# Optimization experiments

Measured on AMD Instinct MI355X. Metric: run time of the kernel, lower is better.

Reference implementation:

```python
import jax, jax.numpy as jnp
import numpy as np

# DPLayer config (init kwargs)
MAX_OP = False            # False -> min-plus (shortest path) semiring; null = +inf
MAKE_POS = True           # GraphLayer make_pos: force positive edge weights
NULL = -1e30 if MAX_OP else 1e30   # finite stand-in for +/-inf (grad-safe)
B, H, W = 512, 256, 256


def setup_inputs() -> dict:
    key = jax.random.key(0)
    images = jax.random.normal(key, (B, 1, H, W), dtype=jnp.float32)
    return {"images": images}


def _edge_weights(images):
    # GraphLayer: edge_f('euclidean') on pixel values, made positive via softplus.
    x = images[:, 0, :, :]                       # [B, H, W] node/edge costs theta
    if MAKE_POS:
        x = jax.nn.softplus(x)
    return x


def _dp(theta):
    # V[i,j] = theta[i,j] + comb(V[i-1,j], V[i-1,j-1], V[i,j-1]); comb = min (max_op=False)
    # Row recurrence is solved in parallel via prefix-sum + associative running-min:
    #   A[j] = comb(V[i-1,j], V[i-1,j-1])
    #   V[i,j] = S[j] + runmin_{k<=j}(A[k] - S[k-1]),  S = cumsum(theta row)
    comb = jnp.maximum if MAX_OP else jnp.minimum
    null = jnp.asarray(NULL, theta.dtype)
    b = theta.shape[0]

    v0 = jnp.cumsum(theta[:, 0, :], axis=-1)     # first row: only right moves

    def row_step(vprev, th_row):                 # vprev: [B,W], th_row: [B,W]
        shifted = jnp.concatenate([jnp.full((b, 1), null, theta.dtype), vprev[:, :-1]], axis=1)
        A = comb(vprev, shifted)                 # best of up / up-left
        S = jnp.cumsum(th_row, axis=-1)
        Sprev = jnp.concatenate([jnp.zeros((b, 1), theta.dtype), S[:, :-1]], axis=1)
        V = S + jax.lax.associative_scan(comb, A - Sprev, axis=-1)
        return V, None

    vlast, _ = jax.lax.scan(row_step, v0, jnp.moveaxis(theta[:, 1:, :], 1, 0))
    return vlast[:, -1]                          # path length to (H-1, W-1), [B]


def reference(images):
    theta = _edge_weights(images)
    fake_lengths = _dp(theta)
    return fake_lengths
```

## Files before the change

### kernel.cpp

```cpp
#include <hip/hip_runtime.h>


#define HH 256
#define WW 256
#define CH 8
#define NCH 32
#define NULLV 1e30f

#define SBAR() __builtin_amdgcn_sched_barrier(0)

template<int CTRL, int ROWM>
__device__ __forceinline__ float dpp_mov(float x, float oldv) {
    return __builtin_bit_cast(float, __builtin_amdgcn_update_dpp(
        __builtin_bit_cast(int, oldv), __builtin_bit_cast(int, x),
        CTRL, ROWM, 0xF, false));
}

__device__ __forceinline__ float wave_iscan_add(float x) {
    x += dpp_mov<0x111, 0xF>(x, 0.0f);
    x += dpp_mov<0x112, 0xF>(x, 0.0f);
    x += dpp_mov<0x114, 0xF>(x, 0.0f);
    x += dpp_mov<0x118, 0xF>(x, 0.0f);
    x += dpp_mov<0x142, 0xA>(x, 0.0f);
    x += dpp_mov<0x143, 0xC>(x, 0.0f);
    return x;
}

__device__ __forceinline__ float wave_iscan_min(float x) {
    x = fminf(x, dpp_mov<0x111, 0xF>(x, NULLV));
    x = fminf(x, dpp_mov<0x112, 0xF>(x, NULLV));
    x = fminf(x, dpp_mov<0x114, 0xF>(x, NULLV));
    x = fminf(x, dpp_mov<0x118, 0xF>(x, NULLV));
    x = fminf(x, dpp_mov<0x142, 0xA>(x, NULLV));
    x = fminf(x, dpp_mov<0x143, 0xC>(x, NULLV));
    return x;
}

__device__ __forceinline__ float softplus_f(float x) {
    float ax = fabsf(x);
    float t  = __expf(-ax);
    return fmaxf(x, 0.0f) + __logf(1.0f + t);
}

__device__ __forceinline__ float4 prep_row(float4 c) {
    float t0 = softplus_f(c.x);
    float t1 = t0 + softplus_f(c.y);
    float t2 = t1 + softplus_f(c.z);
    float t3 = t2 + softplus_f(c.w);
    float s    = wave_iscan_add(t3);
    float soff = dpp_mov<0x138, 0xF>(s, 0.0f);
    return make_float4(soff + t0, soff + t1, soff + t2, soff + t3);
}

template<int NR>
__device__ __forceinline__ void prep_run(const float4* gp, int row0,
                                         float* b0, float* b1, int lane) {
    float4 L0, L1, L2;
    L0 = gp[(size_t)(row0 + 0) * 64];
    if constexpr (NR > 1) L1 = gp[(size_t)(row0 + 1) * 64];
    if constexpr (NR > 2) L2 = gp[(size_t)(row0 + 2) * 64];
    SBAR();
    for (int k = 0; k < NCH; ++k) {
        float4 N0 = L0, N1 = L1, N2 = L2;
        if (k + 1 < NCH) {
            const size_t rn = (size_t)(k + 1) * CH + row0;
            N0 = gp[(rn + 0) * 64];
            if constexpr (NR > 1) N1 = gp[(rn + 1) * 64];
            if constexpr (NR > 2) N2 = gp[(rn + 2) * 64];
        }
        SBAR();
        float* buf = (k & 1) ? b1 : b0;
        *reinterpret_cast<float4*>(&buf[0 * WW + lane * 4]) = prep_row(L0);
        if constexpr (NR > 1)
            *reinterpret_cast<float4*>(&buf[1 * WW + lane * 4]) = prep_row(L1);
        if constexpr (NR > 2)
            *reinterpret_cast<float4*>(&buf[2 * WW + lane * 4]) = prep_row(L2);
        __syncthreads();
        L0 = N0; L1 = N1; L2 = N2;
    }
}

__global__ __launch_bounds__(512, 1) void dp_kernel(const float* __restrict__ img,
                                                    float* __restrict__ out) {
    const int tid = threadIdx.x;
    const int wid = tid >> 6;
    const int lane = tid & 63;

    __shared__ __align__(16) float sbuf[2][2][CH][WW];

    if (wid < 2) {
        const int imgi = wid;
        __builtin_amdgcn_s_setprio(1);
        float v0, v1, v2, v3;

        auto row_step = [&](const float4& S) {
            float soff = dpp_mov<0x138, 0xF>(S.w, 0.0f);
            float vm1  = dpp_mov<0x138, 0xF>(v3, NULLV);
            float B0 = fminf(v0, vm1) - soff;
            float B1 = fminf(v1, v0) - S.x;
            float B2 = fminf(v2, v1) - S.y;
            float B3 = fminf(v3, v2) - S.z;
            float m1 = fminf(B0, B1);
            float m2 = fminf(m1, B2);
            float m3 = fminf(m2, B3);
            float mm   = wave_iscan_min(m3);
            float moff = dpp_mov<0x138, 0xF>(mm, NULLV);
            v0 = S.x + fminf(moff, B0);
            v1 = S.y + fminf(moff, m1);
            v2 = S.z + fminf(moff, m2);
            v3 = S.w + fminf(moff, m3);
        };

#define RD(buf, i) (*reinterpret_cast<const float4*>(&(buf)[i][lane * 4]))
        __syncthreads();
        {
            const float(*buf)[WW] = sbuf[imgi][0];
            float4 R0 = RD(buf, 0), R1 = RD(buf, 1), R2 = RD(buf, 2),
                   R3 = RD(buf, 3), R4 = RD(buf, 4), R5 = RD(buf, 5),
                   R6 = RD(buf, 6), R7 = RD(buf, 7);
            v0 = R0.x; v1 = R0.y; v2 = R0.z; v3 = R0.w;
            row_step(R1); row_step(R2); row_step(R3); row_step(R4);
            row_step(R5); row_step(R6); row_step(R7);
        }
        for (int k = 1; k < NCH; ++k) {
            __syncthreads();
            const float(*buf)[WW] = sbuf[imgi][k & 1];
            float4 R0 = RD(buf, 0), R1 = RD(buf, 1), R2 = RD(buf, 2),
                   R3 = RD(buf, 3), R4 = RD(buf, 4), R5 = RD(buf, 5),
                   R6 = RD(buf, 6), R7 = RD(buf, 7);
            row_step(R0); row_step(R1); row_step(R2); row_step(R3);
            row_step(R4); row_step(R5); row_step(R6); row_step(R7);
        }
#undef RD
        if (lane == 63) out[2 * blockIdx.x + imgi] = v3;
    } else {
        const int imgi = (wid - 2) & 1;
        const int pw   = (wid - 2) >> 1;
        const float* gbase = img + (size_t)(2 * blockIdx.x + imgi) * HH * WW;
        const float4* gp = reinterpret_cast<const float4*>(gbase) + lane;
        const int row0 = pw * 3;
        float* b0 = &sbuf[imgi][0][row0][0];
        float* b1 = &sbuf[imgi][1][row0][0];
        if (pw < 2) prep_run<3>(gp, row0, b0, b1, lane);
        else        prep_run<2>(gp, row0, b0, b1, lane);
    }
}

extern "C" void kernel_launch(void* const* d_in, const int* in_sizes, int n_in,
                              void* d_out, int out_size, void* d_ws, size_t ws_size,
                              hipStream_t stream) {
    const float* img = (const float*)d_in[0];
    float* out = (float*)d_out;
    dp_kernel<<<out_size / 2, 512, 0, stream>>>(img, out);
}
```

Baseline: 45.19 us.

## Enlarge DP row chunks to 32 rows and software-pipeline LDS reads

```diff
diff --git a/kernel.cpp b/kernel.cpp
--- a/kernel.cpp
+++ b/kernel.cpp
@@ -3,8 +3,8 @@
 
 #define HH 256
 #define WW 256
-#define CH 8
-#define NCH 32
+#define CH 32
+#define NCH 8
 #define NULLV 1e30f
 
 #define SBAR() __builtin_amdgcn_sched_barrier(0)
@@ -55,28 +55,27 @@
 template<int NR>
 __device__ __forceinline__ void prep_run(const float4* gp, int row0,
                                          float* b0, float* b1, int lane) {
-    float4 L0, L1, L2;
-    L0 = gp[(size_t)(row0 + 0) * 64];
-    if constexpr (NR > 1) L1 = gp[(size_t)(row0 + 1) * 64];
-    if constexpr (NR > 2) L2 = gp[(size_t)(row0 + 2) * 64];
+    float4 L[NR];
+#pragma unroll
+    for (int i = 0; i < NR; ++i) L[i] = gp[(size_t)(row0 + i) * 64];
     SBAR();
     for (int k = 0; k < NCH; ++k) {
-        float4 N0 = L0, N1 = L1, N2 = L2;
+        float4 N[NR];
+#pragma unroll
+        for (int i = 0; i < NR; ++i) N[i] = L[i];
         if (k + 1 < NCH) {
             const size_t rn = (size_t)(k + 1) * CH + row0;
-            N0 = gp[(rn + 0) * 64];
-            if constexpr (NR > 1) N1 = gp[(rn + 1) * 64];
-            if constexpr (NR > 2) N2 = gp[(rn + 2) * 64];
+#pragma unroll
+            for (int i = 0; i < NR; ++i) N[i] = gp[(rn + i) * 64];
         }
         SBAR();
         float* buf = (k & 1) ? b1 : b0;
-        *reinterpret_cast<float4*>(&buf[0 * WW + lane * 4]) = prep_row(L0);
-        if constexpr (NR > 1)
-            *reinterpret_cast<float4*>(&buf[1 * WW + lane * 4]) = prep_row(L1);
-        if constexpr (NR > 2)
-            *reinterpret_cast<float4*>(&buf[2 * WW + lane * 4]) = prep_row(L2);
+#pragma unroll
+        for (int i = 0; i < NR; ++i)
+            *reinterpret_cast<float4*>(&buf[i * WW + lane * 4]) = prep_row(L[i]);
         __syncthreads();
-        L0 = N0; L1 = N1; L2 = N2;
+#pragma unroll
+        for (int i = 0; i < NR; ++i) L[i] = N[i];
     }
 }
 
@@ -111,38 +110,59 @@
             v3 = S.w + fminf(moff, m3);
         };
 
-#define RD(buf, i) (*reinterpret_cast<const float4*>(&(buf)[i][lane * 4]))
+#define RD8(P, buf, r0)                                                  \
+    P##0 = *reinterpret_cast<const float4*>(&(buf)[(r0) + 0][lane * 4]); \
+    P##1 = *reinterpret_cast<const float4*>(&(buf)[(r0) + 1][lane * 4]); \
+    P##2 = *reinterpret_cast<const float4*>(&(buf)[(r0) + 2][lane * 4]); \
+    P##3 = *reinterpret_cast<const float4*>(&(buf)[(r0) + 3][lane * 4]); \
+    P##4 = *reinterpret_cast<const float4*>(&(buf)[(r0) + 4][lane * 4]); \
+    P##5 = *reinterpret_cast<const float4*>(&(buf)[(r0) + 5][lane * 4]); \
+    P##6 = *reinterpret_cast<const float4*>(&(buf)[(r0) + 6][lane * 4]); \
+    P##7 = *reinterpret_cast<const float4*>(&(buf)[(r0) + 7][lane * 4]);
+#define ST8(P)                                                           \
+    row_step(P##0); row_step(P##1); row_step(P##2); row_step(P##3);      \
+    row_step(P##4); row_step(P##5); row_step(P##6); row_step(P##7);
+
+        float4 A0, A1, A2, A3, A4, A5, A6, A7;
+        float4 B0, B1, B2, B3, B4, B5, B6, B7;
+
         __syncthreads();
         {
             const float(*buf)[WW] = sbuf[imgi][0];
-            float4 R0 = RD(buf, 0), R1 = RD(buf, 1), R2 = RD(buf, 2),
-                   R3 = RD(buf, 3), R4 = RD(buf, 4), R5 = RD(buf, 5),
-                   R6 = RD(buf, 6), R7 = RD(buf, 7);
-            v0 = R0.x; v1 = R0.y; v2 = R0.z; v3 = R0.w;
-            row_step(R1); row_step(R2); row_step(R3); row_step(R4);
-            row_step(R5); row_step(R6); row_step(R7);
+            RD8(A, buf, 0); RD8(B, buf, 8);
+            v0 = A0.x; v1 = A0.y; v2 = A0.z; v3 = A0.w;
+            row_step(A1); row_step(A2); row_step(A3);
+            row_step(A4); row_step(A5); row_step(A6); row_step(A7);
+            RD8(A, buf, 16);
+            ST8(B);
+            RD8(B, buf, 24);
+            ST8(A);
+            ST8(B);
         }
         for (int k = 1; k < NCH; ++k) {
             __syncthreads();
             const float(*buf)[WW] = sbuf[imgi][k & 1];
-            float4 R0 = RD(buf, 0), R1 = RD(buf, 1), R2 = RD(buf, 2),
-                   R3 = RD(buf, 3), R4 = RD(buf, 4), R5 = RD(buf, 5),
-                   R6 = RD(buf, 6), R7 = RD(buf, 7);
-            row_step(R0); row_step(R1); row_step(R2); row_step(R3);
-            row_step(R4); row_step(R5); row_step(R6); row_step(R7);
+            RD8(A, buf, 0); RD8(B, buf, 8);
+            ST8(A);
+            RD8(A, buf, 16);
+            ST8(B);
+            RD8(B, buf, 24);
+            ST8(A);
+            ST8(B);
         }
-#undef RD
+#undef RD8
+#undef ST8
         if (lane == 63) out[2 * blockIdx.x + imgi] = v3;
     } else {
         const int imgi = (wid - 2) & 1;
         const int pw   = (wid - 2) >> 1;
         const float* gbase = img + (size_t)(2 * blockIdx.x + imgi) * HH * WW;
         const float4* gp = reinterpret_cast<const float4*>(gbase) + lane;
-        const int row0 = pw * 3;
+        const int row0 = pw * 11;
         float* b0 = &sbuf[imgi][0][row0][0];
         float* b1 = &sbuf[imgi][1][row0][0];
-        if (pw < 2) prep_run<3>(gp, row0, b0, b1, lane);
-        else        prep_run<2>(gp, row0, b0, b1, lane);
+        if (pw < 2) prep_run<11>(gp, row0, b0, b1, lane);
+        else        prep_run<10>(gp, row0, b0, b1, lane);
     }
 }
 
```

After: 46.03 us. No clear change (+1.8%).
